# Kernel tuning notes

Hardware: AMD Instinct MI355X
Metric: run time of the kernel (lower is better)

## Reference

```python
import jax, jax.numpy as jnp
import numpy as np

KERNEL_SIZE = 7
NUM_HEADS = 16
CHANNELS = 1024
HEAD_DIM = CHANNELS // NUM_HEADS
PAD = KERNEL_SIZE // 2


def setup_inputs() -> dict:
    key = jax.random.key(0)
    k1, k2 = jax.random.split(key)
    B, S, C = 4, 2048, CHANNELS
    x = jax.random.normal(k1, (B, S, C), dtype=jnp.float32)
    W_pred = jax.random.normal(k2, (C, KERNEL_SIZE * NUM_HEADS), dtype=jnp.float32) * (1.0 / np.sqrt(C))
    b_pred = jnp.zeros((KERNEL_SIZE * NUM_HEADS,), dtype=jnp.float32)
    return {"x": x, "W_pred": W_pred, "b_pred": b_pred}


def reference(x, W_pred, b_pred):
    B, S, C = x.shape
    # per-position kernel prediction: [B,S,H,K]
    kernels = (jnp.einsum('bsc,ck->bsk', x, W_pred) + b_pred).reshape(B, S, NUM_HEADS, KERNEL_SIZE)
    # split channels into heads: [B,S,H,D]
    x_heads = x.reshape(B, S, NUM_HEADS, HEAD_DIM)
    # pad along sequence dim
    x_pad = jnp.pad(x_heads, ((0, 0), (PAD, PAD), (0, 0), (0, 0)))
    # sum over K shifted slices weighted by predicted kernels (K is small, fixed)
    out = jnp.zeros_like(x_heads)
    for i in range(KERNEL_SIZE):
        out = out + kernels[:, :, :, i:i + 1] * jax.lax.dynamic_slice_in_dim(x_pad, i, S, axis=1)
    return out.reshape(B, S, C)
```

## Files before the change

### kernel.cpp

```cpp
#include <hip/hip_runtime.h>
#include <hip/hip_bf16.h>
#include <cstdint>

#define SEQ   2048
#define CH    1024
#define NHEAD 16
#define KSZ   7
#define NCOL  112
#define PADW  3

#define BM       16
#define NTHREADS 256
#define LDK_STR  113
#define NKSTEP   32
#define WS_FRAG_BYTES (NKSTEP * 7 * 64 * 16)

typedef __bf16 v8bf __attribute__((ext_vector_type(8)));
typedef float  v4f  __attribute__((ext_vector_type(4)));

__global__ __launch_bounds__(256)
void prep_w(const float* __restrict__ Wp, __bf16* __restrict__ wsB) {
    const int g  = blockIdx.x * 256 + threadIdx.x;
    const int j  = g & 7;
    const int l  = (g >> 3) & 63;
    const int st = g >> 9;
    const int s  = st / 7;
    const int t  = st - s * 7;
    const int k  = s * 32 + (l >> 4) * 8 + j;
    const int n  = t * 16 + (l & 15);
    wsB[g] = (__bf16)Wp[k * NCOL + n];
}

template <bool PRE>
__global__ __launch_bounds__(NTHREADS, 2)
void dynconv_fused(const float* __restrict__ x,
                   const float* __restrict__ Wp,
                   const float* __restrict__ bp,
                   const __bf16* __restrict__ wsB,
                   float* __restrict__ out)
{
    __shared__ float ldsK[BM * LDK_STR];

    const int tid  = threadIdx.x;
    const int bb   = blockIdx.x;
    const int b    = bb >> 7;
    const int s0   = (bb & 127) << 4;

    const int wave = tid >> 6;
    const int lane = tid & 63;
    const int lq   = lane >> 4;
    const int lm   = lane & 15;

    const float* xbase = x + (size_t)b * SEQ * CH;

    const int tile0 = wave * 2;
    const int tile1 = (wave < 3) ? wave * 2 + 1 : 6;

    v4f acc0 = (v4f){0.f, 0.f, 0.f, 0.f};
    v4f acc1 = (v4f){0.f, 0.f, 0.f, 0.f};

    const float* arow = xbase + (size_t)(s0 + lm) * CH + lq * 8;

    #pragma unroll 8
    for (int s = 0; s < NKSTEP; ++s) {
        const float* p = arow + s * 32;
        const v4f v0 = *(const v4f*)p;
        const v4f v1 = *(const v4f*)(p + 4);
        v8bf af;
        af[0] = (__bf16)v0.x; af[1] = (__bf16)v0.y;
        af[2] = (__bf16)v0.z; af[3] = (__bf16)v0.w;
        af[4] = (__bf16)v1.x; af[5] = (__bf16)v1.y;
        af[6] = (__bf16)v1.z; af[7] = (__bf16)v1.w;

        v8bf bf0, bf1;
        if (PRE) {
            bf0 = *(const v8bf*)&wsB[(size_t)((s * 7 + tile0) * 64 + lane) * 8];
            bf1 = *(const v8bf*)&wsB[(size_t)((s * 7 + tile1) * 64 + lane) * 8];
        } else {
            #pragma unroll
            for (int j = 0; j < 8; ++j) {
                const int k = s * 32 + lq * 8 + j;
                bf0[j] = (__bf16)Wp[k * NCOL + tile0 * 16 + lm];
                bf1[j] = (__bf16)Wp[k * NCOL + tile1 * 16 + lm];
            }
        }
        acc0 = __builtin_amdgcn_mfma_f32_16x16x32_bf16(af, bf0, acc0, 0, 0, 0);
        acc1 = __builtin_amdgcn_mfma_f32_16x16x32_bf16(af, bf1, acc1, 0, 0, 0);
    }

    {
        const int ct0 = tile0 * 16 + lm;
        const float bias0 = bp[ct0];
        #pragma unroll
        for (int r = 0; r < 4; ++r)
            ldsK[(lq * 4 + r) * LDK_STR + ct0] = acc0[r] + bias0;
        if (wave < 3) {
            const int ct1 = tile1 * 16 + lm;
            const float bias1 = bp[ct1];
            #pragma unroll
            for (int r = 0; r < 4; ++r)
                ldsK[(lq * 4 + r) * LDK_STR + ct1] = acc1[r] + bias1;
        }
    }

    const int h  = tid >> 4;
    const int c4 = tid << 2;

    v4f win[BM + 6];
    #pragma unroll
    for (int i = 0; i < BM + 6; ++i) {
        const int sg = s0 - PADW + i;
        win[i] = (sg >= 0 && sg < SEQ)
                     ? *(const v4f*)(xbase + (size_t)sg * CH + c4)
                     : (v4f){0.f, 0.f, 0.f, 0.f};
    }

    __syncthreads();

    float* orow = out + ((size_t)b * SEQ + s0) * CH + c4;
    #pragma unroll
    for (int r = 0; r < BM; ++r) {
        const float* kp = &ldsK[r * LDK_STR + h * KSZ];
        v4f a = (v4f){0.f, 0.f, 0.f, 0.f};
        #pragma unroll
        for (int i = 0; i < KSZ; ++i) {
            a += kp[i] * win[r + i];
        }
        *(v4f*)(orow + (size_t)r * CH) = a;
    }
}

extern "C" void kernel_launch(void* const* d_in, const int* in_sizes, int n_in,
                              void* d_out, int out_size, void* d_ws, size_t ws_size,
                              hipStream_t stream) {
    const float* x  = (const float*)d_in[0];
    const float* Wp = (const float*)d_in[1];
    const float* bp = (const float*)d_in[2];
    float* out = (float*)d_out;

    if (ws_size >= (size_t)WS_FRAG_BYTES) {
        __bf16* wsB = (__bf16*)d_ws;
        prep_w<<<dim3(448), dim3(256), 0, stream>>>(Wp, wsB);
        dynconv_fused<true><<<dim3(512), dim3(NTHREADS), 0, stream>>>(x, Wp, bp, wsB, out);
    } else {
        dynconv_fused<false><<<dim3(512), dim3(NTHREADS), 0, stream>>>(x, Wp, bp, nullptr, out);
    }
}
```

Measured before the change: 105.2 us.

## Split fused kernel into separate GEMM and dynamic-conv kernels via workspace buffer

The single fused kernel, which both computed the predicted kernels with MFMA and applied the convolution, is split in two. The first kernel writes the per-position kernels to a global workspace buffer. The second runs the convolution with 8-row tiles over 1024 blocks and uses nontemporal stores. The aim is more parallelism and occupancy in the bandwidth-bound conv stage, paid for with an extra kernel launch and a write plus read of the roughly 3.6 MB kernel buffer, and the new path requires a larger workspace.

```diff
diff --git a/kernel.cpp b/kernel.cpp
--- a/kernel.cpp
+++ b/kernel.cpp
@@ -9,11 +9,15 @@
 #define NCOL  112
 #define PADW  3
 
-#define BM       16
 #define NTHREADS 256
-#define LDK_STR  113
 #define NKSTEP   32
-#define WS_FRAG_BYTES (NKSTEP * 7 * 64 * 16)
+
+#define WSB_BYTES   (NKSTEP * 7 * 64 * 16)
+#define KBUF_OFF    262144
+#define KBUF_BYTES  (4 * SEQ * NCOL * 4)
+#define WS_NEEDED   (KBUF_OFF + KBUF_BYTES)
+
+#define BM2      8
 
 typedef __bf16 v8bf __attribute__((ext_vector_type(8)));
 typedef float  v4f  __attribute__((ext_vector_type(4)));
@@ -31,16 +35,12 @@
     wsB[g] = (__bf16)Wp[k * NCOL + n];
 }
 
-template <bool PRE>
-__global__ __launch_bounds__(NTHREADS, 2)
-void dynconv_fused(const float* __restrict__ x,
-                   const float* __restrict__ Wp,
-                   const float* __restrict__ bp,
-                   const __bf16* __restrict__ wsB,
-                   float* __restrict__ out)
+__global__ __launch_bounds__(NTHREADS)
+void gemm_kernels(const float* __restrict__ x,
+                  const __bf16* __restrict__ wsB,
+                  const float* __restrict__ bp,
+                  float* __restrict__ Kbuf)
 {
-    __shared__ float ldsK[BM * LDK_STR];
-
     const int tid  = threadIdx.x;
     const int bb   = blockIdx.x;
     const int b    = bb >> 7;
@@ -51,15 +51,13 @@
     const int lq   = lane >> 4;
     const int lm   = lane & 15;
 
-    const float* xbase = x + (size_t)b * SEQ * CH;
-
     const int tile0 = wave * 2;
     const int tile1 = (wave < 3) ? wave * 2 + 1 : 6;
 
     v4f acc0 = (v4f){0.f, 0.f, 0.f, 0.f};
     v4f acc1 = (v4f){0.f, 0.f, 0.f, 0.f};
 
-    const float* arow = xbase + (size_t)(s0 + lm) * CH + lq * 8;
+    const float* arow = x + ((size_t)b * SEQ + s0 + lm) * CH + lq * 8;
 
     #pragma unroll 8
     for (int s = 0; s < NKSTEP; ++s) {
@@ -72,60 +70,143 @@
         af[4] = (__bf16)v1.x; af[5] = (__bf16)v1.y;
         af[6] = (__bf16)v1.z; af[7] = (__bf16)v1.w;
 
+        const v8bf bf0 = *(const v8bf*)&wsB[(size_t)((s * 7 + tile0) * 64 + lane) * 8];
+        const v8bf bf1 = *(const v8bf*)&wsB[(size_t)((s * 7 + tile1) * 64 + lane) * 8];
+
+        acc0 = __builtin_amdgcn_mfma_f32_16x16x32_bf16(af, bf0, acc0, 0, 0, 0);
+        acc1 = __builtin_amdgcn_mfma_f32_16x16x32_bf16(af, bf1, acc1, 0, 0, 0);
+    }
+
+    float* krow = Kbuf + (size_t)(b * SEQ + s0) * NCOL;
+    {
+        const int ct0 = tile0 * 16 + lm;
+        const float bias0 = bp[ct0];
+        #pragma unroll
+        for (int r = 0; r < 4; ++r)
+            krow[(size_t)(lq * 4 + r) * NCOL + ct0] = acc0[r] + bias0;
+    }
+    if (wave < 3) {
+        const int ct1 = tile1 * 16 + lm;
+        const float bias1 = bp[ct1];
+        #pragma unroll
+        for (int r = 0; r < 4; ++r)
+            krow[(size_t)(lq * 4 + r) * NCOL + ct1] = acc1[r] + bias1;
+    }
+}
+
+__global__ __launch_bounds__(NTHREADS)
+void dynconv(const float* __restrict__ x,
+             const float* __restrict__ Kbuf,
+             float* __restrict__ out)
+{
+    __shared__ float ldsK[BM2 * NCOL];
+
+    const int tid = threadIdx.x;
+    const int bb  = blockIdx.x;
+    const int b   = bb >> 8;
+    const int s0  = (bb & 255) << 3;
+
+    const float* kb = Kbuf + (size_t)(b * SEQ + s0) * NCOL;
+    if (tid < 224) {
+        const v4f kv = *(const v4f*)(kb + tid * 4);
+        *(v4f*)(&ldsK[tid * 4]) = kv;
+    }
+
+    const int h  = tid >> 4;
+    const int c4 = tid << 2;
+    const float* xb = x + (size_t)b * SEQ * CH + c4;
+
+    v4f win[BM2 + 6];
+    #pragma unroll
+    for (int i = 0; i < BM2 + 6; ++i) {
+        const int sg = s0 - PADW + i;
+        win[i] = (sg >= 0 && sg < SEQ) ? *(const v4f*)(xb + (size_t)sg * CH)
+                                       : (v4f){0.f, 0.f, 0.f, 0.f};
+    }
+
+    __syncthreads();
+
+    float* ob = out + ((size_t)b * SEQ + s0) * CH + c4;
+    #pragma unroll
+    for (int r = 0; r < BM2; ++r) {
+        const float* kp = &ldsK[r * NCOL + h * KSZ];
+        v4f a = (v4f){0.f, 0.f, 0.f, 0.f};
+        #pragma unroll
+        for (int i = 0; i < KSZ; ++i) {
+            a += kp[i] * win[r + i];
+        }
+        __builtin_nontemporal_store(a, (v4f*)(ob + (size_t)r * CH));
+    }
+}
+
+__global__ __launch_bounds__(NTHREADS, 2)
+void dynconv_fused_fb(const float* __restrict__ x,
+                      const float* __restrict__ Wp,
+                      const float* __restrict__ bp,
+                      float* __restrict__ out)
+{
+    __shared__ float ldsK[16 * 113];
+    const int tid  = threadIdx.x;
+    const int bb   = blockIdx.x;
+    const int b    = bb >> 7;
+    const int s0   = (bb & 127) << 4;
+    const int wave = tid >> 6;
+    const int lane = tid & 63;
+    const int lq   = lane >> 4;
+    const int lm   = lane & 15;
+    const float* xbase = x + (size_t)b * SEQ * CH;
+    const int tile0 = wave * 2;
+    const int tile1 = (wave < 3) ? wave * 2 + 1 : 6;
+    v4f acc0 = (v4f){0.f,0.f,0.f,0.f};
+    v4f acc1 = (v4f){0.f,0.f,0.f,0.f};
+    const float* arow = xbase + (size_t)(s0 + lm) * CH + lq * 8;
+    #pragma unroll 8
+    for (int s = 0; s < NKSTEP; ++s) {
+        const float* p = arow + s * 32;
+        const v4f v0 = *(const v4f*)p;
+        const v4f v1 = *(const v4f*)(p + 4);
+        v8bf af;
+        af[0]=(__bf16)v0.x; af[1]=(__bf16)v0.y; af[2]=(__bf16)v0.z; af[3]=(__bf16)v0.w;
+        af[4]=(__bf16)v1.x; af[5]=(__bf16)v1.y; af[6]=(__bf16)v1.z; af[7]=(__bf16)v1.w;
         v8bf bf0, bf1;
-        if (PRE) {
-            bf0 = *(const v8bf*)&wsB[(size_t)((s * 7 + tile0) * 64 + lane) * 8];
-            bf1 = *(const v8bf*)&wsB[(size_t)((s * 7 + tile1) * 64 + lane) * 8];
-        } else {
-            #pragma unroll
-            for (int j = 0; j < 8; ++j) {
-                const int k = s * 32 + lq * 8 + j;
-                bf0[j] = (__bf16)Wp[k * NCOL + tile0 * 16 + lm];
-                bf1[j] = (__bf16)Wp[k * NCOL + tile1 * 16 + lm];
-            }
+        #pragma unroll
+        for (int j = 0; j < 8; ++j) {
+            const int k = s * 32 + lq * 8 + j;
+            bf0[j] = (__bf16)Wp[k * NCOL + tile0 * 16 + lm];
+            bf1[j] = (__bf16)Wp[k * NCOL + tile1 * 16 + lm];
         }
         acc0 = __builtin_amdgcn_mfma_f32_16x16x32_bf16(af, bf0, acc0, 0, 0, 0);
         acc1 = __builtin_amdgcn_mfma_f32_16x16x32_bf16(af, bf1, acc1, 0, 0, 0);
     }
-
     {
         const int ct0 = tile0 * 16 + lm;
         const float bias0 = bp[ct0];
         #pragma unroll
-        for (int r = 0; r < 4; ++r)
-            ldsK[(lq * 4 + r) * LDK_STR + ct0] = acc0[r] + bias0;
+        for (int r = 0; r < 4; ++r) ldsK[(lq*4+r)*113 + ct0] = acc0[r] + bias0;
         if (wave < 3) {
             const int ct1 = tile1 * 16 + lm;
             const float bias1 = bp[ct1];
             #pragma unroll
-            for (int r = 0; r < 4; ++r)
-                ldsK[(lq * 4 + r) * LDK_STR + ct1] = acc1[r] + bias1;
+            for (int r = 0; r < 4; ++r) ldsK[(lq*4+r)*113 + ct1] = acc1[r] + bias1;
         }
     }
-
     const int h  = tid >> 4;
     const int c4 = tid << 2;
-
-    v4f win[BM + 6];
-    #pragma unroll
-    for (int i = 0; i < BM + 6; ++i) {
+    v4f win[22];
+    #pragma unroll
+    for (int i = 0; i < 22; ++i) {
         const int sg = s0 - PADW + i;
-        win[i] = (sg >= 0 && sg < SEQ)
-                     ? *(const v4f*)(xbase + (size_t)sg * CH + c4)
-                     : (v4f){0.f, 0.f, 0.f, 0.f};
-    }
-
+        win[i] = (sg >= 0 && sg < SEQ) ? *(const v4f*)(xbase + (size_t)sg * CH + c4)
+                                       : (v4f){0.f,0.f,0.f,0.f};
+    }
     __syncthreads();
-
     float* orow = out + ((size_t)b * SEQ + s0) * CH + c4;
     #pragma unroll
-    for (int r = 0; r < BM; ++r) {
-        const float* kp = &ldsK[r * LDK_STR + h * KSZ];
-        v4f a = (v4f){0.f, 0.f, 0.f, 0.f};
-        #pragma unroll
-        for (int i = 0; i < KSZ; ++i) {
-            a += kp[i] * win[r + i];
-        }
+    for (int r = 0; r < 16; ++r) {
+        const float* kp = &ldsK[r * 113 + h * KSZ];
+        v4f a = (v4f){0.f,0.f,0.f,0.f};
+        #pragma unroll
+        for (int i = 0; i < KSZ; ++i) a += kp[i] * win[r + i];
         *(v4f*)(orow + (size_t)r * CH) = a;
     }
 }
@@ -138,11 +219,13 @@
     const float* bp = (const float*)d_in[2];
     float* out = (float*)d_out;
 
-    if (ws_size >= (size_t)WS_FRAG_BYTES) {
-        __bf16* wsB = (__bf16*)d_ws;
+    if (ws_size >= (size_t)WS_NEEDED) {
+        __bf16* wsB  = (__bf16*)d_ws;
+        float*  Kbuf = (float*)((char*)d_ws + KBUF_OFF);
         prep_w<<<dim3(448), dim3(256), 0, stream>>>(Wp, wsB);
-        dynconv_fused<true><<<dim3(512), dim3(NTHREADS), 0, stream>>>(x, Wp, bp, wsB, out);
+        gemm_kernels<<<dim3(512), dim3(NTHREADS), 0, stream>>>(x, wsB, bp, Kbuf);
+        dynconv<<<dim3(1024), dim3(NTHREADS), 0, stream>>>(x, Kbuf, out);
     } else {
-        dynconv_fused<false><<<dim3(512), dim3(NTHREADS), 0, stream>>>(x, Wp, bp, nullptr, out);
-    }
-}
+        dynconv_fused_fb<<<dim3(512), dim3(NTHREADS), 0, stream>>>(x, Wp, bp, out);
+    }
+}
```

Result: slower. 111.5 us (+5.9%).
